# Kernel tuning notes

Measured on AMD Instinct MI355X. Metric: run time of the kernel, lower is better.

## Reference

```python
import jax, jax.numpy as jnp
import numpy as np

EPS = 1e-8            # EpisodicMemory.eps
TEMPERATURE = 0.25    # default temperature in query()


def setup_inputs() -> dict:
    key = jax.random.key(0)
    k1, k2, k3 = jax.random.split(key, 3)
    B, N, KD, VD, TOPK = 512, 500000, 128, 64, 16
    queries = jax.random.normal(k1, (B, KD), dtype=jnp.float32)
    # stored keys are L2-normalized at insert time
    keys = jax.random.normal(k2, (N, KD), dtype=jnp.float32)
    keys = keys / jnp.clip(jnp.linalg.norm(keys, axis=1, keepdims=True), EPS, None)
    values = jax.random.normal(k3, (N, VD), dtype=jnp.float32)
    return {"queries": queries, "keys": keys, "values": values, "topk": TOPK}


def reference(queries, keys, values, topk):
    # cosine similarity: normalize queries (keys already normalized in memory)
    qn = queries / jnp.clip(jnp.linalg.norm(queries, axis=1, keepdims=True), EPS, None)
    scores = (qn @ keys.T) / max(1e-6, TEMPERATURE)          # [B, N]
    topv, topidx = jax.lax.top_k(scores, topk)               # [B, K], [B, K]
    # stable exp-softmax with eps in the denominator (as in torch source)
    topv_exp = jnp.exp(topv - jnp.max(topv, axis=1, keepdims=True))
    topw = topv_exp / (jnp.sum(topv_exp, axis=1, keepdims=True) + EPS)
    vals = values[topidx]                                    # gather: [B, K, VD]
    retrieved = jnp.einsum('bk,bkd->bd', topw, vals)         # [B, VD]
    return retrieved, topw, topidx
```

## Files before the change

kernel.cpp:

```cpp
#include <hip/hip_runtime.h>
#include <hip/hip_bf16.h>

#define NB 512
#define KD 128
#define VD 64
#define NKEYS 500000
#define TOPK 16
#define CH 1024
#define NCHUNK 489
#define NCAND (NCHUNK*4)
#define CBUF 64

typedef __attribute__((ext_vector_type(8))) short bf8s;
typedef __attribute__((ext_vector_type(4))) float f4;

__device__ __forceinline__ unsigned f2bf(float x) {
  union { float f; unsigned u; } v; v.f = x;
  return (v.u + 0x7fffu + ((v.u >> 16) & 1u)) >> 16;
}

__device__ __forceinline__ void barrier_lgkm() {
  asm volatile("s_waitcnt lgkmcnt(0)" ::: "memory");
  __builtin_amdgcn_s_barrier();
}

__global__ __launch_bounds__(128) void qnorm_kernel(const float* __restrict__ q,
                                                    float* __restrict__ qn_f,
                                                    short* __restrict__ qn_bf) {
  int b = blockIdx.x, t = threadIdx.x;
  float x = q[b*KD + t];
  float s = x * x;
  #pragma unroll
  for (int o = 32; o > 0; o >>= 1) s += __shfl_down(s, o);
  __shared__ float p[2];
  if ((t & 63) == 0) p[t >> 6] = s;
  __syncthreads();
  float norm = sqrtf(p[0] + p[1]);
  norm = fmaxf(norm, 1e-8f);
  float v = x * (4.0f / norm);
  qn_f[b*KD + t] = v;
  qn_bf[b*KD + t] = (short)f2bf(v);
}

__global__ __launch_bounds__(256) void score_filter_kernel(
    const float* __restrict__ keys, const short* __restrict__ qn_bf,
    float* __restrict__ cand_val, int* __restrict__ cand_idx) {
  __shared__ float slds[256 * 17];
  const int chunk = blockIdx.x, gy = blockIdx.y;
  const int tid  = threadIdx.x;
  const int wave = tid >> 6, lane = tid & 63;
  const int col  = lane & 15, quad = lane >> 4;

  bf8s afrag[4][4];
  const int qbase = gy*256 + wave*64;
  #pragma unroll
  for (int mt = 0; mt < 4; mt++)
    #pragma unroll
    for (int ks = 0; ks < 4; ks++)
      afrag[mt][ks] = *(const bf8s*)(qn_bf + (qbase + mt*16 + col)*KD + ks*32 + quad*8);

  float tv0=-1e30f, tv1=-1e30f, tv2=-1e30f, tv3=-1e30f;
  int   ti0=0, ti1=0, ti2=0, ti3=0;
  const int nchunk0 = chunk * CH;

  f4 x0[4], x1[4];
  {
    int r = nchunk0 + col; if (r > NKEYS-1) r = NKEYS-1;
    const float* kp = keys + (size_t)r*KD + quad*8;
    #pragma unroll
    for (int ks = 0; ks < 4; ks++) {
      x0[ks] = *(const f4*)(kp + ks*32);
      x1[ks] = *(const f4*)(kp + ks*32 + 4);
    }
  }

  for (int nt = 0; nt < CH/16; nt++) {
    const int nb = nchunk0 + nt*16;
    bf8s bfrag[4];
    #pragma unroll
    for (int ks = 0; ks < 4; ks++) {
      bf8s tt;
      tt[0]=(short)f2bf(x0[ks][0]); tt[1]=(short)f2bf(x0[ks][1]);
      tt[2]=(short)f2bf(x0[ks][2]); tt[3]=(short)f2bf(x0[ks][3]);
      tt[4]=(short)f2bf(x1[ks][0]); tt[5]=(short)f2bf(x1[ks][1]);
      tt[6]=(short)f2bf(x1[ks][2]); tt[7]=(short)f2bf(x1[ks][3]);
      bfrag[ks] = tt;
    }
    if (nt + 1 < CH/16) {
      int r = nb + 16 + col; if (r > NKEYS-1) r = NKEYS-1;
      const float* kp = keys + (size_t)r*KD + quad*8;
      #pragma unroll
      for (int ks = 0; ks < 4; ks++) {
        x0[ks] = *(const f4*)(kp + ks*32);
        x1[ks] = *(const f4*)(kp + ks*32 + 4);
      }
    }
    f4 acc[4];
    #pragma unroll
    for (int mt = 0; mt < 4; mt++) { acc[mt][0]=0.f; acc[mt][1]=0.f; acc[mt][2]=0.f; acc[mt][3]=0.f; }
    #pragma unroll
    for (int ks = 0; ks < 4; ks++)
      #pragma unroll
      for (int mt = 0; mt < 4; mt++)
        acc[mt] = __builtin_amdgcn_mfma_f32_16x16x32_bf16(afrag[mt][ks], bfrag[ks], acc[mt], 0, 0, 0);
    #pragma unroll
    for (int mt = 0; mt < 4; mt++)
      #pragma unroll
      for (int rg = 0; rg < 4; rg++)
        slds[(wave*64 + mt*16 + quad*4 + rg)*17 + col] = acc[mt][rg];
    barrier_lgkm();
    #pragma unroll
    for (int c = 0; c < 16; c++) {
      int n = nb + c;
      float v = slds[tid*17 + c];
      if (v > tv3 && n < NKEYS) {
        if (v > tv0)      { tv3=tv2;ti3=ti2; tv2=tv1;ti2=ti1; tv1=tv0;ti1=ti0; tv0=v;ti0=n; }
        else if (v > tv1) { tv3=tv2;ti3=ti2; tv2=tv1;ti2=ti1; tv1=v;ti1=n; }
        else if (v > tv2) { tv3=tv2;ti3=ti2; tv2=v;ti2=n; }
        else              { tv3=v;ti3=n; }
      }
    }
    barrier_lgkm();
  }
  const int gq = gy*256 + tid;
  const size_t o = ((size_t)gq*NCHUNK + chunk)*4;
  cand_val[o+0]=tv0; cand_val[o+1]=tv1; cand_val[o+2]=tv2; cand_val[o+3]=tv3;
  cand_idx[o+0]=ti0; cand_idx[o+1]=ti1; cand_idx[o+2]=ti2; cand_idx[o+3]=ti3;
}

__global__ __launch_bounds__(256) void merge_rescore_kernel(
    const float* __restrict__ qn_f, const float* __restrict__ keys,
    const float* __restrict__ values, const float* __restrict__ cand_val,
    const int* __restrict__ cand_idx, float* __restrict__ out) {
  const int b = blockIdx.x, t = threadIdx.x;
  const int lane = t & 63, wave = t >> 6;
  __shared__ float qs[KD];
  __shared__ unsigned hist[256];
  __shared__ int wtot[4];
  __shared__ int s_bound, s_above, s_bcnt, s_cnt;
  __shared__ float rv[CBUF]; __shared__ int ri[CBUF];
  __shared__ float sval[TOPK]; __shared__ int sidx[TOPK]; __shared__ float sw[TOPK];

  if (t < KD) qs[t] = qn_f[b*KD + t];

  unsigned u[8]; int id[8];
  #pragma unroll
  for (int j = 0; j < 8; j++) {
    int i = t + j*256;
    if (i < NCAND) {
      union { float f; unsigned q; } cvt; cvt.f = cand_val[(size_t)b*NCAND + i];
      unsigned m = cvt.q;
      m = (m & 0x80000000u) ? ~m : (m | 0x80000000u);
      u[j] = m; id[j] = cand_idx[(size_t)b*NCAND + i];
    } else { u[j] = 0u; id[j] = -1; }
  }

  unsigned prefix = 0; int above = 0; unsigned thr = 0; bool done = false;
  #pragma unroll 1
  for (int pass = 0; pass < 3 && !done; pass++) {
    const int shift = 24 - 8*pass;
    hist[t] = 0u;
    __syncthreads();
    #pragma unroll
    for (int j = 0; j < 8; j++) {
      bool ok = (pass == 0) || ((u[j] >> (shift + 8)) == prefix);
      if (ok) atomicAdd(&hist[(u[j] >> shift) & 255u], 1u);
    }
    __syncthreads();
    int h = (int)hist[t];
    int s = h;
    #pragma unroll
    for (int o = 1; o < 64; o <<= 1) {
      int nv = __shfl_down(s, o);
      if (lane + o < 64) s += nv;
    }
    if (lane == 0) wtot[wave] = s;
    __syncthreads();
    int add = 0;
    for (int g = wave + 1; g < 4; g++) add += wtot[g];
    int S = s + add;
    if (above + S >= 32 && above + S - h < 32) {
      s_bound = t; s_above = above + S - h; s_bcnt = h;
    }
    __syncthreads();
    prefix = (prefix << 8) | (unsigned)s_bound;
    above  = s_above;
    if (s_above + s_bcnt <= CBUF || pass == 2) { thr = prefix << shift; done = true; }
    __syncthreads();
  }

  if (t == 0) s_cnt = 0;
  __syncthreads();
  #pragma unroll
  for (int j = 0; j < 8; j++) {
    if (id[j] >= 0 && u[j] >= thr) {
      int p = atomicAdd(&s_cnt, 1);
      if (p < CBUF) ri[p] = id[j];
    }
  }
  __syncthreads();
  const int C = min(s_cnt, CBUF);
  if (t >= C && t < CBUF) ri[t] = 0x7fffffff;
  __syncthreads();

  {
    int c = t >> 2, dg = t & 3;
    float part = 0.f;
    if (c < C) {
      const float* kr = keys + (size_t)ri[c]*KD + dg*32;
      #pragma unroll
      for (int j = 0; j < 32; j++) part += kr[j] * qs[dg*32 + j];
    }
    part += __shfl_down(part, 2, 4);
    part += __shfl_down(part, 1, 4);
    if (dg == 0) rv[c] = (c < C) ? part : -1e30f;
  }
  __syncthreads();

  if (t < CBUF) {
    float v = rv[t]; int idx = ri[t];
    int rank = 0;
    for (int j = 0; j < CBUF; j++) {
      float vj = rv[j]; int ij = ri[j];
      rank += (vj > v) || (vj == v && ij < idx);
    }
    if (rank < TOPK) { sval[rank] = v; sidx[rank] = idx; }
  }
  __syncthreads();

  if (t < TOPK) {
    float m = sval[0];
    float e = expf(sval[t] - m);
    float s2 = e;
    #pragma unroll
    for (int o = 8; o > 0; o >>= 1) s2 += __shfl_down(s2, o, 16);
    s2 = __shfl(s2, 0, 16);
    float w = e / (s2 + 1e-8f);
    sw[t] = w;
    out[NB*VD + b*TOPK + t] = w;
    out[NB*VD + NB*TOPK + b*TOPK + t] = (float)sidx[t];
  }
  __syncthreads();

  if (t < VD) {
    float acc = 0.f;
    #pragma unroll
    for (int k = 0; k < TOPK; k++) acc += sw[k] * values[(size_t)sidx[k]*VD + t];
    out[b*VD + t] = acc;
  }
}

extern "C" void kernel_launch(void* const* d_in, const int* in_sizes, int n_in,
                              void* d_out, int out_size, void* d_ws, size_t ws_size,
                              hipStream_t stream) {
  const float* queries = (const float*)d_in[0];
  const float* keys    = (const float*)d_in[1];
  const float* values  = (const float*)d_in[2];
  float* out = (float*)d_out;

  char* ws = (char*)d_ws;
  float* qn_f  = (float*)ws;
  short* qn_bf = (short*)(ws + (size_t)NB*KD*4);
  float* cand_val = (float*)(ws + (size_t)NB*KD*4 + (size_t)NB*KD*2);
  int*   cand_idx = (int*)((char*)cand_val + (size_t)NB*NCHUNK*4*sizeof(float));

  qnorm_kernel<<<NB, KD, 0, stream>>>(queries, qn_f, qn_bf);
  score_filter_kernel<<<dim3(NCHUNK, 2), 256, 0, stream>>>(keys, qn_bf, cand_val, cand_idx);
  merge_rescore_kernel<<<NB, 256, 0, stream>>>(qn_f, keys, values, cand_val, cand_idx, out);
}
```

Before: 638.1 us.

## Split key chunks across waves and drop per-tile barriers in score filter

The score kernel now gives each block 64 queries and lets its four waves scan disjoint 256-key slices of a chunk independently. This removes the two block barriers per 16-key tile. The per-wave top-4 lists are then merged in LDS into a top-8 per chunk and written as vector stores. A swizzled 1D grid groups the query groups that share a key chunk, so key reads can hit in L2. The cost is twice as many candidates for the merge kernel, which now reads and histograms 16 per thread, and four times more blocks for the score kernel.

```diff
diff --git a/kernel.cpp b/kernel.cpp
--- a/kernel.cpp
+++ b/kernel.cpp
@@ -8,20 +8,18 @@
 #define TOPK 16
 #define CH 1024
 #define NCHUNK 489
-#define NCAND (NCHUNK*4)
+#define CPC 8
+#define NCAND (NCHUNK*CPC)
 #define CBUF 64
+#define JCAND 16
 
 typedef __attribute__((ext_vector_type(8))) short bf8s;
 typedef __attribute__((ext_vector_type(4))) float f4;
+typedef __attribute__((ext_vector_type(4))) int i4;
 
 __device__ __forceinline__ unsigned f2bf(float x) {
   union { float f; unsigned u; } v; v.f = x;
   return (v.u + 0x7fffu + ((v.u >> 16) & 1u)) >> 16;
-}
-
-__device__ __forceinline__ void barrier_lgkm() {
-  asm volatile("s_waitcnt lgkmcnt(0)" ::: "memory");
-  __builtin_amdgcn_s_barrier();
 }
 
 __global__ __launch_bounds__(128) void qnorm_kernel(const float* __restrict__ q,
@@ -45,14 +43,17 @@
 __global__ __launch_bounds__(256) void score_filter_kernel(
     const float* __restrict__ keys, const short* __restrict__ qn_bf,
     float* __restrict__ cand_val, int* __restrict__ cand_idx) {
-  __shared__ float slds[256 * 17];
-  const int chunk = blockIdx.x, gy = blockIdx.y;
+  __shared__ float slds[4*64*17];
+  const int bid = blockIdx.x;
+  const int chunk = (bid & 7) + 8*(bid >> 6);
+  const int gy    = (bid >> 3) & 7;
+  if (chunk >= NCHUNK) return;
   const int tid  = threadIdx.x;
   const int wave = tid >> 6, lane = tid & 63;
   const int col  = lane & 15, quad = lane >> 4;
 
   bf8s afrag[4][4];
-  const int qbase = gy*256 + wave*64;
+  const int qbase = gy*64;
   #pragma unroll
   for (int mt = 0; mt < 4; mt++)
     #pragma unroll
@@ -61,11 +62,11 @@
 
   float tv0=-1e30f, tv1=-1e30f, tv2=-1e30f, tv3=-1e30f;
   int   ti0=0, ti1=0, ti2=0, ti3=0;
-  const int nchunk0 = chunk * CH;
+  const int k0 = chunk*CH + wave*256;
 
   f4 x0[4], x1[4];
   {
-    int r = nchunk0 + col; if (r > NKEYS-1) r = NKEYS-1;
+    int r = k0 + col; if (r > NKEYS-1) r = NKEYS-1;
     const float* kp = keys + (size_t)r*KD + quad*8;
     #pragma unroll
     for (int ks = 0; ks < 4; ks++) {
@@ -74,8 +75,9 @@
     }
   }
 
-  for (int nt = 0; nt < CH/16; nt++) {
-    const int nb = nchunk0 + nt*16;
+  #pragma unroll 1
+  for (int t16 = 0; t16 < 16; t16++) {
+    const int nb = k0 + t16*16;
     bf8s bfrag[4];
     #pragma unroll
     for (int ks = 0; ks < 4; ks++) {
@@ -86,7 +88,7 @@
       tt[6]=(short)f2bf(x1[ks][2]); tt[7]=(short)f2bf(x1[ks][3]);
       bfrag[ks] = tt;
     }
-    if (nt + 1 < CH/16) {
+    if (t16 < 15) {
       int r = nb + 16 + col; if (r > NKEYS-1) r = NKEYS-1;
       const float* kp = keys + (size_t)r*KD + quad*8;
       #pragma unroll
@@ -107,12 +109,11 @@
     for (int mt = 0; mt < 4; mt++)
       #pragma unroll
       for (int rg = 0; rg < 4; rg++)
-        slds[(wave*64 + mt*16 + quad*4 + rg)*17 + col] = acc[mt][rg];
-    barrier_lgkm();
+        slds[wave*1088 + (mt*16 + quad*4 + rg)*17 + col] = acc[mt][rg];
     #pragma unroll
     for (int c = 0; c < 16; c++) {
       int n = nb + c;
-      float v = slds[tid*17 + c];
+      float v = slds[wave*1088 + lane*17 + c];
       if (v > tv3 && n < NKEYS) {
         if (v > tv0)      { tv3=tv2;ti3=ti2; tv2=tv1;ti2=ti1; tv1=tv0;ti1=ti0; tv0=v;ti0=n; }
         else if (v > tv1) { tv3=tv2;ti3=ti2; tv2=tv1;ti2=ti1; tv1=v;ti1=n; }
@@ -120,12 +121,45 @@
         else              { tv3=v;ti3=n; }
       }
     }
-    barrier_lgkm();
-  }
-  const int gq = gy*256 + tid;
-  const size_t o = ((size_t)gq*NCHUNK + chunk)*4;
-  cand_val[o+0]=tv0; cand_val[o+1]=tv1; cand_val[o+2]=tv2; cand_val[o+3]=tv3;
-  cand_idx[o+0]=ti0; cand_idx[o+1]=ti1; cand_idx[o+2]=ti2; cand_idx[o+3]=ti3;
+  }
+
+  __syncthreads();
+  float* fv = slds;
+  int*   fi = (int*)(slds + 1024);
+  const int pb = wave*256 + lane*4;
+  fv[pb+0]=tv0; fv[pb+1]=tv1; fv[pb+2]=tv2; fv[pb+3]=tv3;
+  fi[pb+0]=ti0; fi[pb+1]=ti1; fi[pb+2]=ti2; fi[pb+3]=ti3;
+  __syncthreads();
+  if (tid < 64) {
+    float bv[8]; int bi[8];
+    #pragma unroll
+    for (int k = 0; k < 8; k++) { bv[k] = -1e30f; bi[k] = 0; }
+    #pragma unroll
+    for (int w = 0; w < 4; w++)
+      #pragma unroll
+      for (int j = 0; j < 4; j++) {
+        float v = fv[w*256 + tid*4 + j];
+        int  ix = fi[w*256 + tid*4 + j];
+        if (v > bv[7]) {
+          bv[7] = v; bi[7] = ix;
+          #pragma unroll
+          for (int s = 7; s > 0; s--)
+            if (bv[s] > bv[s-1]) {
+              float tv = bv[s]; bv[s] = bv[s-1]; bv[s-1] = tv;
+              int   ti = bi[s]; bi[s] = bi[s-1]; bi[s-1] = ti;
+            }
+        }
+      }
+    const size_t o = ((size_t)(qbase + tid)*NCHUNK + chunk)*CPC;
+    f4 v0; v0[0]=bv[0]; v0[1]=bv[1]; v0[2]=bv[2]; v0[3]=bv[3];
+    f4 v1; v1[0]=bv[4]; v1[1]=bv[5]; v1[2]=bv[6]; v1[3]=bv[7];
+    i4 j0; j0[0]=bi[0]; j0[1]=bi[1]; j0[2]=bi[2]; j0[3]=bi[3];
+    i4 j1; j1[0]=bi[4]; j1[1]=bi[5]; j1[2]=bi[6]; j1[3]=bi[7];
+    *(f4*)(cand_val + o)     = v0;
+    *(f4*)(cand_val + o + 4) = v1;
+    *(i4*)(cand_idx + o)     = j0;
+    *(i4*)(cand_idx + o + 4) = j1;
+  }
 }
 
 __global__ __launch_bounds__(256) void merge_rescore_kernel(
@@ -143,9 +177,9 @@
 
   if (t < KD) qs[t] = qn_f[b*KD + t];
 
-  unsigned u[8]; int id[8];
+  unsigned u[JCAND]; int id[JCAND];
   #pragma unroll
-  for (int j = 0; j < 8; j++) {
+  for (int j = 0; j < JCAND; j++) {
     int i = t + j*256;
     if (i < NCAND) {
       union { float f; unsigned q; } cvt; cvt.f = cand_val[(size_t)b*NCAND + i];
@@ -162,7 +196,7 @@
     hist[t] = 0u;
     __syncthreads();
     #pragma unroll
-    for (int j = 0; j < 8; j++) {
+    for (int j = 0; j < JCAND; j++) {
       bool ok = (pass == 0) || ((u[j] >> (shift + 8)) == prefix);
       if (ok) atomicAdd(&hist[(u[j] >> shift) & 255u], 1u);
     }
@@ -192,7 +226,7 @@
   if (t == 0) s_cnt = 0;
   __syncthreads();
   #pragma unroll
-  for (int j = 0; j < 8; j++) {
+  for (int j = 0; j < JCAND; j++) {
     if (id[j] >= 0 && u[j] >= thr) {
       int p = atomicAdd(&s_cnt, 1);
       if (p < CBUF) ri[p] = id[j];
@@ -262,9 +296,9 @@
   float* qn_f  = (float*)ws;
   short* qn_bf = (short*)(ws + (size_t)NB*KD*4);
   float* cand_val = (float*)(ws + (size_t)NB*KD*4 + (size_t)NB*KD*2);
-  int*   cand_idx = (int*)((char*)cand_val + (size_t)NB*NCHUNK*4*sizeof(float));
+  int*   cand_idx = (int*)((char*)cand_val + (size_t)NB*NCAND*sizeof(float));
 
   qnorm_kernel<<<NB, KD, 0, stream>>>(queries, qn_f, qn_bf);
-  score_filter_kernel<<<dim3(NCHUNK, 2), 256, 0, stream>>>(keys, qn_bf, cand_val, cand_idx);
+  score_filter_kernel<<<62*64, 256, 0, stream>>>(keys, qn_bf, cand_val, cand_idx);
   merge_rescore_kernel<<<NB, 256, 0, stream>>>(qn_f, keys, values, cand_val, cand_idx, out);
 }
```

Result: no change. 628.9 us (-1.4%).
